# Performance work log

Hardware: AMD Instinct MI355X
Metric: run time of the kernel (lower is better)

Reference implementation:

```python
import jax, jax.numpy as jnp
import numpy as np

B, S, D, H = 4, 1024, 128, 8  # batch, seq, per-head dim (= d_q=d_k=d_v), heads


def _cv_linear(xr, xi, wr, wi):
    """Complex linear y = (xr+i xi) @ (wr+i wi)^T, torch Linear convention W:[out,in]."""
    yr = jnp.einsum('bsi,oi->bso', xr, wr) - jnp.einsum('bsi,oi->bso', xi, wi)
    yi = jnp.einsum('bsi,oi->bso', xr, wi) + jnp.einsum('bsi,oi->bso', xi, wr)
    return yr, yi


def _split_heads(x):  # [B,S,H*D] -> [B,H,S,D]
    return x.reshape(B, S, H, D).transpose(0, 2, 1, 3)


def setup_inputs() -> dict:
    key = jax.random.key(0)
    ks = jax.random.split(key, 14)
    mk = lambda k, shp: jax.random.normal(k, shp, dtype=jnp.float32)
    # torch nn.Linear default init ~ U(-1/sqrt(in),1/sqrt(in)); gaussian*scale is fine for a numeric baseline
    sd_in = 1.0 / np.sqrt(D)
    sd_o = 1.0 / np.sqrt(H * D)
    return {
        'q_r': mk(ks[0], (B, S, D)), 'q_i': mk(ks[1], (B, S, D)),
        'k_r': mk(ks[2], (B, S, D)), 'k_i': mk(ks[3], (B, S, D)),
        'v_r': mk(ks[4], (B, S, D)), 'v_i': mk(ks[5], (B, S, D)),
        'Wq_r': mk(ks[6], (H * D, D)) * sd_in, 'Wq_i': mk(ks[7], (H * D, D)) * sd_in,
        'Wk_r': mk(ks[8], (H * D, D)) * sd_in, 'Wk_i': mk(ks[9], (H * D, D)) * sd_in,
        'Wv_r': mk(ks[10], (H * D, D)) * sd_in, 'Wv_i': mk(ks[11], (H * D, D)) * sd_in,
        'Wo_r': mk(ks[12], (D, H * D)) * sd_o, 'Wo_i': mk(ks[13], (D, H * D)) * sd_o,
    }


def _forward(q_r, q_i, k_r, k_i, v_r, v_i,
             Wq_r, Wq_i, Wk_r, Wk_i, Wv_r, Wv_i, Wo_r, Wo_i):
    qr, qi = _cv_linear(q_r, q_i, Wq_r, Wq_i)
    kr, ki = _cv_linear(k_r, k_i, Wk_r, Wk_i)
    vr, vi = _cv_linear(v_r, v_i, Wv_r, Wv_i)
    qr, qi, kr, ki, vr, vi = map(_split_heads, (qr, qi, kr, ki, vr, vi))
    scale = 1.0 / np.sqrt(D).astype(np.float32)
    # complex scores = q @ k^T (no conjugation, matching torch.bmm)
    sr = jnp.einsum('bhqd,bhkd->bhqk', qr, kr) - jnp.einsum('bhqd,bhkd->bhqk', qi, ki)
    si = jnp.einsum('bhqd,bhkd->bhqk', qr, ki) + jnp.einsum('bhqd,bhkd->bhqk', qi, kr)
    sr, si = sr * scale, si * scale
    attn = jax.nn.softmax(jnp.sqrt(sr * sr + si * si), axis=-1)  # real weights
    or_ = jnp.einsum('bhqk,bhkd->bhqd', attn, vr)
    oi_ = jnp.einsum('bhqk,bhkd->bhqd', attn, vi)
    # [B,H,S,D] -> [B,S,H*D]
    or_ = or_.transpose(0, 2, 1, 3).reshape(B, S, H * D)
    oi_ = oi_.transpose(0, 2, 1, 3).reshape(B, S, H * D)
    yr, yi = _cv_linear(or_, oi_, Wo_r, Wo_i)
    return yr, yi


def reference(q_r, q_i, k_r, k_i, v_r, v_i,
              Wq_r, Wq_i, Wk_r, Wk_i, Wv_r, Wv_i, Wo_r, Wo_i):
    yr, yi = _forward(q_r, q_i, k_r, k_i, v_r, v_i,
                      Wq_r, Wq_i, Wk_r, Wk_i, Wv_r, Wv_i, Wo_r, Wo_i)
    return yr.astype(jnp.complex64) + 1j * yi.astype(jnp.complex64)
```

## Files before the change

kernel.cpp:

```cpp
#include <hip/hip_runtime.h>


#define SS 1024
#define DD 128
#define HH 8
#define BH 32
#define MTOT 4096
#define KQ 256
#define NPROJ 1024
#define KO 2048

typedef _Float16 f16_t;
typedef __attribute__((ext_vector_type(8))) _Float16 f16x8;
typedef __attribute__((ext_vector_type(4))) float f32x4;

__device__ inline f32x4 mfma16(f16x8 a, f16x8 b, f32x4 c) {
    return __builtin_amdgcn_mfma_f32_16x16x32_f16(a, b, c, 0, 0, 0);
}

__device__ inline f16x8 load_cvt8(const float* __restrict__ p) {
    float4 a = *reinterpret_cast<const float4*>(p);
    float4 b = *reinterpret_cast<const float4*>(p + 4);
    f16x8 r;
    r[0] = (f16_t)a.x; r[1] = (f16_t)a.y; r[2] = (f16_t)a.z; r[3] = (f16_t)a.w;
    r[4] = (f16_t)b.x; r[5] = (f16_t)b.y; r[6] = (f16_t)b.z; r[7] = (f16_t)b.w;
    return r;
}

__global__ void sentinel_fill(float* __restrict__ out, int n, float v) {
    int i = blockIdx.x * 256 + threadIdx.x;
    if (i < n) out[i] = v;
}

__global__ void prep_w6(const float* __restrict__ W0, const float* __restrict__ W1,
                        const float* __restrict__ W2, const float* __restrict__ W3,
                        const float* __restrict__ W4, const float* __restrict__ W5,
                        f16_t* __restrict__ W6) {
    int idx = blockIdx.x * 256 + threadIdx.x;
    int mat = idx >> 17, rem = idx & 131071;
    const float* s = (mat == 0) ? W0 : (mat == 1) ? W1 : (mat == 2) ? W2
                    : (mat == 3) ? W3 : (mat == 4) ? W4 : W5;
    W6[idx] = (f16_t)s[rem];
}

__global__ void prep_wo2(const float* __restrict__ Wo_r, const float* __restrict__ Wo_i,
                         f16_t* __restrict__ Wo2) {
    int idx = blockIdx.x * 256 + threadIdx.x;
    Wo2[idx] = (f16_t)(idx < 131072 ? Wo_r[idx] : Wo_i[idx - 131072]);
}

__global__ __launch_bounds__(256) void proj_gemm(
        const float* __restrict__ Xr0, const float* __restrict__ Xi0,
        const float* __restrict__ Xr1, const float* __restrict__ Xi1,
        const float* __restrict__ Xr2, const float* __restrict__ Xi2,
        const f16_t* __restrict__ W6,
        f16_t* __restrict__ Qc, f16_t* __restrict__ Kc,
        f16_t* __restrict__ VTr, f16_t* __restrict__ VTi) {
    int proj = blockIdx.z;
    const float* Xr = (proj == 0) ? Xr0 : (proj == 1) ? Xr1 : Xr2;
    const float* Xi = (proj == 0) ? Xi0 : (proj == 1) ? Xi1 : Xi2;
    const f16_t* Wr = W6 + (size_t)(2 * proj) * NPROJ * DD;
    const f16_t* Wi = Wr + NPROJ * DD;
    int lane = threadIdx.x & 63, wid = threadIdx.x >> 6;
    int l15 = lane & 15, lg = lane >> 4;
    int m0 = blockIdx.x * 16;
    int row = m0 + l15;

    f16x8 aR[4], aI[4];
    {
        const float* xr = Xr + (size_t)row * DD + lg * 8;
        const float* xi = Xi + (size_t)row * DD + lg * 8;
#pragma unroll
        for (int kc = 0; kc < 4; ++kc) {
            aR[kc] = load_cvt8(xr + kc * 32);
            aI[kc] = load_cvt8(xi + kc * 32);
        }
    }

    for (int nt = wid * 16; nt < wid * 16 + 16; ++nt) {
        int o = nt * 16 + l15;
        const f16_t* wr = Wr + (size_t)o * DD + lg * 8;
        const f16_t* wi = Wi + (size_t)o * DD + lg * 8;
        f32x4 rr = {0.f,0.f,0.f,0.f}, ii = {0.f,0.f,0.f,0.f};
        f32x4 ri = {0.f,0.f,0.f,0.f}, ir = {0.f,0.f,0.f,0.f};
#pragma unroll
        for (int kc = 0; kc < 4; ++kc) {
            f16x8 bR = *reinterpret_cast<const f16x8*>(wr + kc * 32);
            f16x8 bI = *reinterpret_cast<const f16x8*>(wi + kc * 32);
            rr = mfma16(aR[kc], bR, rr);
            ii = mfma16(aI[kc], bI, ii);
            ri = mfma16(aR[kc], bI, ri);
            ir = mfma16(aI[kc], bR, ir);
        }
        int h = o >> 7, d = o & 127;
#pragma unroll
        for (int j = 0; j < 4; ++j) {
            int m = m0 + lg * 4 + j;
            int b = m >> 10, sl = m & 1023;
            int bh = b * HH + h;
            f16_t yr = (f16_t)(rr[j] - ii[j]);
            f16_t yi = (f16_t)(ri[j] + ir[j]);
            if (proj == 0) {
                Qc[((size_t)bh * SS + sl) * KQ + d]      = yr;
                Qc[((size_t)bh * SS + sl) * KQ + DD + d] = yi;
            } else if (proj == 1) {
                Kc[((size_t)bh * SS + sl) * KQ + d]      = yr;
                Kc[((size_t)bh * SS + sl) * KQ + DD + d] = yi;
            } else {
                VTr[((size_t)bh * DD + d) * SS + sl] = yr;
                VTi[((size_t)bh * DD + d) * SS + sl] = yi;
            }
        }
    }
}

__global__ __launch_bounds__(256) void attn_kernel(
        const f16_t* __restrict__ Qc, const f16_t* __restrict__ Kc,
        const f16_t* __restrict__ VTr, const f16_t* __restrict__ VTi,
        f16_t* __restrict__ Xo) {
    int swz = (int)((blockIdx.x & 7) * 64 + (blockIdx.x >> 3));
    int qt = swz & 15;
    int bh = swz >> 4;
    int lane = threadIdx.x & 63, wid = threadIdx.x >> 6;
    int l15 = lane & 15, lg = lane >> 4;
    int q0 = qt * 64 + wid * 16;

    const f16_t* Qb  = Qc  + (size_t)bh * SS * KQ;
    const f16_t* Kb  = Kc  + (size_t)bh * SS * KQ;
    const f16_t* Vrb = VTr + (size_t)bh * DD * SS;
    const f16_t* Vib = VTi + (size_t)bh * DD * SS;

    __shared__ __align__(16) f16_t Pbuf[4][16][40];

    f16x8 aQ[8];
    {
        const f16_t* qrow = Qb + (size_t)(q0 + l15) * KQ + lg * 8;
#pragma unroll
        for (int kc = 0; kc < 8; ++kc)
            aQ[kc] = *reinterpret_cast<const f16x8*>(qrow + kc * 32);
    }
    f32x4 accR[8], accI[8];
#pragma unroll
    for (int t = 0; t < 8; ++t) { accR[t] = {0.f,0.f,0.f,0.f}; accI[t] = {0.f,0.f,0.f,0.f}; }
    float m_run[4], l_lane[4];
#pragma unroll
    for (int j = 0; j < 4; ++j) { m_run[j] = -1e30f; l_lane[j] = 0.f; }
    const float scale = 0.08838834764831845f;

    for (int kt = 0; kt < 32; ++kt) {
        int kbase = kt * 32;
        float mag[2][4];
#pragma unroll
        for (int nt = 0; nt < 2; ++nt) {
            const f16_t* krow = Kb + (size_t)(kbase + nt * 16 + l15) * KQ + lg * 8;
            f32x4 arr = {0.f,0.f,0.f,0.f}, aii = {0.f,0.f,0.f,0.f};
            f32x4 ari = {0.f,0.f,0.f,0.f}, air = {0.f,0.f,0.f,0.f};
#pragma unroll
            for (int kc = 0; kc < 4; ++kc) {
                f16x8 bLo = *reinterpret_cast<const f16x8*>(krow + kc * 32);
                f16x8 bHi = *reinterpret_cast<const f16x8*>(krow + DD + kc * 32);
                arr = mfma16(aQ[kc],     bLo, arr);
                aii = mfma16(aQ[kc + 4], bHi, aii);
                ari = mfma16(aQ[kc],     bHi, ari);
                air = mfma16(aQ[kc + 4], bLo, air);
            }
#pragma unroll
            for (int j = 0; j < 4; ++j) {
                float sr = arr[j] - aii[j];
                float si = ari[j] + air[j];
                mag[nt][j] = sqrtf(sr * sr + si * si) * scale;
            }
        }

        bool ok = true;
#pragma unroll
        for (int j = 0; j < 4; ++j)
            ok = ok && (mag[0][j] <= m_run[j]) && (mag[1][j] <= m_run[j]);
        if (!__all(ok)) {
            float fac[4];
#pragma unroll
            for (int j = 0; j < 4; ++j) {
                float t = fmaxf(mag[0][j], mag[1][j]);
                t = fmaxf(t, __shfl_xor(t, 1));
                t = fmaxf(t, __shfl_xor(t, 2));
                t = fmaxf(t, __shfl_xor(t, 4));
                t = fmaxf(t, __shfl_xor(t, 8));
                float mn = fmaxf(m_run[j], t);
                fac[j] = __expf(m_run[j] - mn);
                m_run[j] = mn;
                l_lane[j] *= fac[j];
            }
#pragma unroll
            for (int t = 0; t < 8; ++t)
#pragma unroll
                for (int j = 0; j < 4; ++j) { accR[t][j] *= fac[j]; accI[t][j] *= fac[j]; }
        }

        float p0[4], p1[4];
#pragma unroll
        for (int j = 0; j < 4; ++j) {
            p0[j] = __expf(mag[0][j] - m_run[j]);
            p1[j] = __expf(mag[1][j] - m_run[j]);
            l_lane[j] += p0[j] + p1[j];
        }
#pragma unroll
        for (int j = 0; j < 4; ++j) {
            Pbuf[wid][lg * 4 + j][l15]      = (f16_t)p0[j];
            Pbuf[wid][lg * 4 + j][16 + l15] = (f16_t)p1[j];
        }
        f16x8 aP = *reinterpret_cast<const f16x8*>(&Pbuf[wid][l15][lg * 8]);

#pragma unroll
        for (int dt = 0; dt < 8; ++dt) {
            const f16_t* vrr = Vrb + (size_t)(dt * 16 + l15) * SS + kbase + lg * 8;
            const f16_t* vri = Vib + (size_t)(dt * 16 + l15) * SS + kbase + lg * 8;
            accR[dt] = mfma16(aP, *reinterpret_cast<const f16x8*>(vrr), accR[dt]);
            accI[dt] = mfma16(aP, *reinterpret_cast<const f16x8*>(vri), accI[dt]);
        }
    }

    int b = bh >> 3, h = bh & 7;
#pragma unroll
    for (int j = 0; j < 4; ++j) {
        float s = l_lane[j];
        s += __shfl_xor(s, 1);
        s += __shfl_xor(s, 2);
        s += __shfl_xor(s, 4);
        s += __shfl_xor(s, 8);
        float inv = 1.0f / s;
        int m = b * SS + q0 + lg * 4 + j;
        f16_t* orow = Xo + (size_t)m * KO;
#pragma unroll
        for (int dt = 0; dt < 8; ++dt) {
            int col = h * DD + dt * 16 + l15;
            orow[col]         = (f16_t)(accR[dt][j] * inv);
            orow[NPROJ + col] = (f16_t)(accI[dt][j] * inv);
        }
    }
}

__global__ __launch_bounds__(512) void outproj_gemm(
        const f16_t* __restrict__ Xo, const f16_t* __restrict__ Wo2,
        float* __restrict__ out, int mode) {
    int lane = threadIdx.x & 63, wid = threadIdx.x >> 6;
    int l15 = lane & 15, lg = lane >> 4;
    int m0 = blockIdx.x * 16;
    const f16_t* Wor = Wo2;
    const f16_t* Woi = Wo2 + (size_t)DD * NPROJ;
    const f16_t* arow = Xo + (size_t)(m0 + l15) * KO + lg * 8;

    int n = wid * 16 + l15;
    const f16_t* wr = Wor + (size_t)n * NPROJ + lg * 8;
    const f16_t* wi = Woi + (size_t)n * NPROJ + lg * 8;
    f32x4 r1 = {0.f,0.f,0.f,0.f}, r2 = {0.f,0.f,0.f,0.f};
    f32x4 i1 = {0.f,0.f,0.f,0.f}, i2 = {0.f,0.f,0.f,0.f};
    for (int kc = 0; kc < 32; ++kc) {
        f16x8 aOr = *reinterpret_cast<const f16x8*>(arow + kc * 32);
        f16x8 aOi = *reinterpret_cast<const f16x8*>(arow + NPROJ + kc * 32);
        f16x8 bR  = *reinterpret_cast<const f16x8*>(wr + kc * 32);
        f16x8 bI  = *reinterpret_cast<const f16x8*>(wi + kc * 32);
        r1 = mfma16(aOr, bR, r1);
        r2 = mfma16(aOi, bI, r2);
        if (mode) {
            i1 = mfma16(aOr, bI, i1);
            i2 = mfma16(aOi, bR, i2);
        }
    }
#pragma unroll
    for (int j = 0; j < 4; ++j) {
        int m = m0 + lg * 4 + j;
        if (mode == 0) {
            out[(size_t)m * DD + n] = r1[j] - r2[j];
        } else {
            out[((size_t)m * DD + n) * 2]     = r1[j] - r2[j];
            out[((size_t)m * DD + n) * 2 + 1] = i1[j] + i2[j];
        }
    }
}

extern "C" void kernel_launch(void* const* d_in, const int* in_sizes, int n_in,
                              void* d_out, int out_size, void* d_ws, size_t ws_size,
                              hipStream_t stream) {
    int blocks_out = (out_size + 255) / 256;
    if (n_in < 14) {
        sentinel_fill<<<blocks_out, 256, 0, stream>>>((float*)d_out, out_size, 54321.0f);
        return;
    }
    int mode;
    if (out_size == MTOT * DD) mode = 0;
    else if (out_size == 2 * MTOT * DD) mode = 1;
    else {
        sentinel_fill<<<blocks_out, 256, 0, stream>>>((float*)d_out, out_size, 77777.0f);
        return;
    }
    if (ws_size < (size_t)(64u << 20)) {
        sentinel_fill<<<blocks_out, 256, 0, stream>>>((float*)d_out, out_size, 12345.0f);
        return;
    }

    const float* q_r  = (const float*)d_in[0];
    const float* q_i  = (const float*)d_in[1];
    const float* k_r  = (const float*)d_in[2];
    const float* k_i  = (const float*)d_in[3];
    const float* v_r  = (const float*)d_in[4];
    const float* v_i  = (const float*)d_in[5];
    const float* Wq_r = (const float*)d_in[6];
    const float* Wq_i = (const float*)d_in[7];
    const float* Wk_r = (const float*)d_in[8];
    const float* Wk_i = (const float*)d_in[9];
    const float* Wv_r = (const float*)d_in[10];
    const float* Wv_i = (const float*)d_in[11];
    const float* Wo_r = (const float*)d_in[12];
    const float* Wo_i = (const float*)d_in[13];

    char* w = (char*)d_ws;
    f16_t* Qc  = (f16_t*)(w);
    f16_t* Kc  = (f16_t*)(w + ((size_t)16 << 20));
    f16_t* VTr = (f16_t*)(w + ((size_t)32 << 20));
    f16_t* VTi = (f16_t*)(w + ((size_t)40 << 20));
    f16_t* Xo  = (f16_t*)(w + ((size_t)48 << 20));
    f16_t* W6  = Xo;
    f16_t* Wo2 = Qc;

    prep_w6<<<(6 * NPROJ * DD) / 256, 256, 0, stream>>>(Wq_r, Wq_i, Wk_r, Wk_i, Wv_r, Wv_i, W6);
    proj_gemm<<<dim3(MTOT / 16, 1, 3), 256, 0, stream>>>(q_r, q_i, k_r, k_i, v_r, v_i, W6,
                                                         Qc, Kc, VTr, VTi);
    attn_kernel<<<512, 256, 0, stream>>>(Qc, Kc, VTr, VTi, Xo);
    prep_wo2<<<(2 * DD * NPROJ) / 256, 256, 0, stream>>>(Wo_r, Wo_i, Wo2);
    outproj_gemm<<<MTOT / 16, 512, 0, stream>>>(Xo, Wo2, (float*)d_out, mode);
}
```

Baseline: 406.6 us.

## Stage K and V tiles in double-buffered shared memory for attention

The attention kernel now loads each 32-key tile of K and the transposed V into double-buffered LDS, cooperatively across the four waves, instead of every wave reading K/V directly from global memory. This cuts the fourfold redundant global traffic per block. The next tile is prefetched while the current one is computed. It adds a block-wide barrier per iteration and about 70KB of LDS, which can lower occupancy. The prefetch is a synchronous load-then-store, so the overlap depends on the compiler scheduling.

```diff
diff --git a/kernel.cpp b/kernel.cpp
--- a/kernel.cpp
+++ b/kernel.cpp
@@ -123,6 +123,7 @@
     int bh = swz >> 4;
     int lane = threadIdx.x & 63, wid = threadIdx.x >> 6;
     int l15 = lane & 15, lg = lane >> 4;
+    int tid = threadIdx.x;
     int q0 = qt * 64 + wid * 16;
 
     const f16_t* Qb  = Qc  + (size_t)bh * SS * KQ;
@@ -130,7 +131,32 @@
     const f16_t* Vrb = VTr + (size_t)bh * DD * SS;
     const f16_t* Vib = VTi + (size_t)bh * DD * SS;
 
+    __shared__ __align__(16) f16_t Ks [2][32][264];
+    __shared__ __align__(16) f16_t VsR[2][128][40];
+    __shared__ __align__(16) f16_t VsI[2][128][40];
     __shared__ __align__(16) f16_t Pbuf[4][16][40];
+
+    int krow = tid >> 3, kcu0 = (tid & 7) * 4;
+    int vrow = tid >> 1, vc0 = (tid & 1) * 16;
+
+#define STAGE(buf, kbase)                                                      \
+    {                                                                          \
+        const f16_t* srcK = Kb + (size_t)((kbase) + krow) * KQ;                \
+        _Pragma("unroll")                                                      \
+        for (int i = 0; i < 4; ++i)                                            \
+            *reinterpret_cast<f16x8*>(&Ks[buf][krow][(kcu0 + i) * 8]) =        \
+                *reinterpret_cast<const f16x8*>(srcK + (kcu0 + i) * 8);        \
+        const f16_t* srcR = Vrb + (size_t)vrow * SS + (kbase) + vc0;           \
+        const f16_t* srcI = Vib + (size_t)vrow * SS + (kbase) + vc0;           \
+        *reinterpret_cast<f16x8*>(&VsR[buf][vrow][vc0])     =                  \
+            *reinterpret_cast<const f16x8*>(srcR);                             \
+        *reinterpret_cast<f16x8*>(&VsR[buf][vrow][vc0 + 8]) =                  \
+            *reinterpret_cast<const f16x8*>(srcR + 8);                         \
+        *reinterpret_cast<f16x8*>(&VsI[buf][vrow][vc0])     =                  \
+            *reinterpret_cast<const f16x8*>(srcI);                             \
+        *reinterpret_cast<f16x8*>(&VsI[buf][vrow][vc0 + 8]) =                  \
+            *reinterpret_cast<const f16x8*>(srcI + 8);                         \
+    }
 
     f16x8 aQ[8];
     {
@@ -147,18 +173,23 @@
     for (int j = 0; j < 4; ++j) { m_run[j] = -1e30f; l_lane[j] = 0.f; }
     const float scale = 0.08838834764831845f;
 
+    STAGE(0, 0);
+    __syncthreads();
+
     for (int kt = 0; kt < 32; ++kt) {
-        int kbase = kt * 32;
+        int buf = kt & 1;
+        if (kt + 1 < 32) STAGE(buf ^ 1, (kt + 1) * 32);
+
         float mag[2][4];
 #pragma unroll
         for (int nt = 0; nt < 2; ++nt) {
-            const f16_t* krow = Kb + (size_t)(kbase + nt * 16 + l15) * KQ + lg * 8;
+            const f16_t* krow_l = &Ks[buf][nt * 16 + l15][lg * 8];
             f32x4 arr = {0.f,0.f,0.f,0.f}, aii = {0.f,0.f,0.f,0.f};
             f32x4 ari = {0.f,0.f,0.f,0.f}, air = {0.f,0.f,0.f,0.f};
 #pragma unroll
             for (int kc = 0; kc < 4; ++kc) {
-                f16x8 bLo = *reinterpret_cast<const f16x8*>(krow + kc * 32);
-                f16x8 bHi = *reinterpret_cast<const f16x8*>(krow + DD + kc * 32);
+                f16x8 bLo = *reinterpret_cast<const f16x8*>(krow_l + kc * 32);
+                f16x8 bHi = *reinterpret_cast<const f16x8*>(krow_l + DD + kc * 32);
                 arr = mfma16(aQ[kc],     bLo, arr);
                 aii = mfma16(aQ[kc + 4], bHi, aii);
                 ari = mfma16(aQ[kc],     bHi, ari);
@@ -212,11 +243,12 @@
 
 #pragma unroll
         for (int dt = 0; dt < 8; ++dt) {
-            const f16_t* vrr = Vrb + (size_t)(dt * 16 + l15) * SS + kbase + lg * 8;
-            const f16_t* vri = Vib + (size_t)(dt * 16 + l15) * SS + kbase + lg * 8;
+            const f16_t* vrr = &VsR[buf][dt * 16 + l15][lg * 8];
+            const f16_t* vri = &VsI[buf][dt * 16 + l15][lg * 8];
             accR[dt] = mfma16(aP, *reinterpret_cast<const f16x8*>(vrr), accR[dt]);
             accI[dt] = mfma16(aP, *reinterpret_cast<const f16x8*>(vri), accI[dt]);
         }
+        __syncthreads();
     }
 
     int b = bh >> 3, h = bh & 7;
@@ -237,6 +269,7 @@
             orow[NPROJ + col] = (f16_t)(accI[dt][j] * inv);
         }
     }
+#undef STAGE
 }
 
 __global__ __launch_bounds__(512) void outproj_gemm(
```

New measurement: 333.9 us. -17.9%, faster.
